# Performance work log

Measured on AMD Instinct MI355X. Metric: run time of the kernel, lower is better.

Reference implementation:

```python
import jax, jax.numpy as jnp
import numpy as np

HIDDEN = 2048
KEY_DIM = 2048
NUM_HEADS = 16
EPS = 1e-05


def rms_norm(x, w, eps=EPS):
    ms = jnp.mean(x * x, axis=-1, keepdims=True)
    return x * jax.lax.rsqrt(ms + eps) * w


def setup_inputs() -> dict:
    key = jax.random.key(0)
    ks = jax.random.split(key, 6)
    bound = 1.0 / np.sqrt(HIDDEN)  # kaiming-uniform-ish scale
    x = jax.random.normal(ks[0], (2, 2048, HIDDEN), dtype=jnp.float32)
    rms_w = jnp.ones((HIDDEN,), dtype=jnp.float32)
    Wq = jax.random.uniform(ks[1], (HIDDEN, KEY_DIM), jnp.float32, -bound, bound)
    Wk = jax.random.uniform(ks[2], (HIDDEN, KEY_DIM), jnp.float32, -bound, bound)
    Wv = jax.random.uniform(ks[3], (HIDDEN, KEY_DIM), jnp.float32, -bound, bound)
    Wo = jax.random.uniform(ks[4], (KEY_DIM, HIDDEN), jnp.float32, -bound, bound)
    return {"x": x, "rms_w": rms_w, "Wq": Wq, "Wk": Wk, "Wv": Wv, "Wo": Wo}


def reference(x, rms_w, Wq, Wk, Wv, Wo):
    B, S, _ = x.shape
    residual = x
    xn = rms_norm(x, rms_w)
    # project and split heads: [B,S,H,Dh]
    q = (xn @ Wq).reshape(B, S, NUM_HEADS, KEY_DIM // NUM_HEADS)
    k = (xn @ Wk).reshape(B, S, NUM_HEADS, KEY_DIM // NUM_HEADS)
    v = (xn @ Wv).reshape(B, S, NUM_HEADS, KEY_DIM // NUM_HEADS)
    # NOTE: original scales by 1/sqrt(key_dim), not head_dim — kept faithful
    scale = 1.0 / jnp.sqrt(jnp.float32(KEY_DIM))
    scores = jnp.einsum('bshd,bthd->bhst', q, k) * scale  # [B,H,S,S]
    causal = jnp.tril(jnp.ones((S, S), dtype=bool))
    scores = jnp.where(causal[None, None], scores, -jnp.inf)
    probs = jax.nn.softmax(scores, axis=-1)  # stable max-subtract internally
    out = jnp.einsum('bhst,bthd->bshd', probs, v).reshape(B, S, KEY_DIM)
    return out @ Wo + residual
```

## Files before the change

kernel.cpp:

```cpp
#include <hip/hip_runtime.h>
#include <math.h>

typedef __attribute__((ext_vector_type(8))) short bf16x8;
typedef __attribute__((ext_vector_type(4))) float f32x4;
typedef __attribute__((ext_vector_type(16))) float f32x16;

#define HID 2048
#define SEQ 2048
#define NH  16
#define DH  128
#define QS_LOG2E 0.0318793607f

__device__ __forceinline__ ushort f2bf(float f) {
  union { float f; unsigned u; } v; v.f = f;
  unsigned r = v.u + 0x7fffu + ((v.u >> 16) & 1u);
  return (ushort)(r >> 16);
}

__device__ __forceinline__ void gload16(const ushort* g, ushort* l) {
  __builtin_amdgcn_global_load_lds((const __attribute__((address_space(1))) void*)g,
                                   (__attribute__((address_space(3))) void*)l,
                                   16, 0, 0);
}

#define VMCNT(n) asm volatile("s_waitcnt vmcnt(" #n ")" ::: "memory")
#define ABAR()   asm volatile("s_barrier" ::: "memory")

__global__ __launch_bounds__(256) void k_prep(const float* __restrict__ W0,
                                              const float* __restrict__ W1,
                                              const float* __restrict__ W2,
                                              const float* __restrict__ W3,
                                              ushort* __restrict__ T0,
                                              ushort* __restrict__ T3,
                                              const float* __restrict__ x,
                                              const float* __restrict__ rw,
                                              ushort* __restrict__ xn) {
  const int z = blockIdx.z;
  if (z < 4) {
    __shared__ float t[32][33];
    const float* W = (z == 0) ? W0 : (z == 1) ? W1 : (z == 2) ? W2 : W3;
    ushort* Wt = (z == 3) ? T3 : (T0 + (size_t)z * 2048 * 2048);
    int n0 = blockIdx.x * 32, k0 = blockIdx.y * 32;
    int tx = threadIdx.x, ty = threadIdx.y;
    for (int i = ty; i < 32; i += 8)
      t[i][tx] = W[(size_t)(k0 + i) * HID + n0 + tx];
    __syncthreads();
    for (int i = ty; i < 32; i += 8)
      Wt[(size_t)(n0 + i) * HID + k0 + tx] = f2bf(t[tx][i]);
  } else {
    const int tid = threadIdx.y * 32 + threadIdx.x;
    const int row = blockIdx.y * 64 + blockIdx.x;
    const float* xr = x + (size_t)row * HID;
    int base = tid * 8;
    float4 a = *(const float4*)(xr + base);
    float4 c = *(const float4*)(xr + base + 4);
    float ss = a.x*a.x + a.y*a.y + a.z*a.z + a.w*a.w
             + c.x*c.x + c.y*c.y + c.z*c.z + c.w*c.w;
    #pragma unroll
    for (int off = 32; off > 0; off >>= 1) ss += __shfl_xor(ss, off);
    __shared__ float red[4];
    if ((tid & 63) == 0) red[tid >> 6] = ss;
    __syncthreads();
    float tot = red[0] + red[1] + red[2] + red[3];
    float sc = rsqrtf(tot * (1.0f / HID) + 1e-5f);
    float4 wa = *(const float4*)(rw + base);
    float4 wc = *(const float4*)(rw + base + 4);
    ushort h[8];
    h[0] = f2bf(a.x * sc * wa.x); h[1] = f2bf(a.y * sc * wa.y);
    h[2] = f2bf(a.z * sc * wa.z); h[3] = f2bf(a.w * sc * wa.w);
    h[4] = f2bf(c.x * sc * wc.x); h[5] = f2bf(c.y * sc * wc.y);
    h[6] = f2bf(c.z * sc * wc.z); h[7] = f2bf(c.w * sc * wc.w);
    int4 pk;
    pk.x = h[0] | ((int)h[1] << 16);
    pk.y = h[2] | ((int)h[3] << 16);
    pk.z = h[4] | ((int)h[5] << 16);
    pk.w = h[6] | ((int)h[7] << 16);
    *(int4*)&xn[(size_t)row * HID + base] = pk;
  }
}

__global__ __launch_bounds__(256, 2) void k_gemm12(const ushort* __restrict__ A,
                                                   const ushort* __restrict__ Bt,
                                                   ushort* __restrict__ obf,
                                                   ushort* __restrict__ vt) {
  constexpr int K = 2048, NR = 64;
  __shared__ ushort lds[4][8192];
  const int tid = threadIdx.x;
  const int lane = tid & 63, w = tid >> 6;
  const int wr = w >> 1, wc = w & 1;
  const int g = lane >> 4, l15 = lane & 15;
  const int bm = blockIdx.y, bn = blockIdx.x;

  f32x4 acc[4][4];
  #pragma unroll
  for (int i = 0; i < 4; ++i)
    #pragma unroll
    for (int j = 0; j < 4; ++j) acc[i][j] = f32x4{0.f, 0.f, 0.f, 0.f};

  const ushort* pA[2];
  const ushort* pB[2];
  #pragma unroll
  for (int L = 0; L < 2; ++L) {
    int row = L * 64 + (tid >> 2);
    int ck = (tid & 3) ^ ((row >> 1) & 3);
    pA[L] = &A[(size_t)(bm * 128 + row) * K + ck * 8];
    pB[L] = &Bt[(size_t)(bn * 128 + row) * K + ck * 8];
  }

  auto STAGE = [&](int slot) {
    ushort* base = lds[slot];
    #pragma unroll
    for (int L = 0; L < 2; ++L) {
      gload16(pA[L], base + L * 2048 + w * 512);
      pA[L] += 32;
    }
    #pragma unroll
    for (int L = 0; L < 2; ++L) {
      gload16(pB[L], base + 4096 + L * 2048 + w * 512);
      pB[L] += 32;
    }
  };

  auto COMP = [&](int slot) {
    const ushort* ra = lds[slot];
    const ushort* rb = ra + 4096;
    bf16x8 aF[4], bF[4];
    #pragma unroll
    for (int i = 0; i < 4; ++i) {
      int row = wr * 64 + i * 16 + l15;
      aF[i] = *(const bf16x8*)&ra[row * 32 + ((g ^ ((row >> 1) & 3)) * 8)];
    }
    #pragma unroll
    for (int j = 0; j < 4; ++j) {
      int row = wc * 64 + j * 16 + l15;
      bF[j] = *(const bf16x8*)&rb[row * 32 + ((g ^ ((row >> 1) & 3)) * 8)];
    }
    __builtin_amdgcn_s_setprio(1);
    #pragma unroll
    for (int i = 0; i < 4; ++i)
      #pragma unroll
      for (int j = 0; j < 4; ++j)
        acc[i][j] = __builtin_amdgcn_mfma_f32_16x16x32_bf16(aF[i], bF[j], acc[i][j], 0, 0, 0);
    __builtin_amdgcn_s_setprio(0);
  };

  STAGE(0); STAGE(1); STAGE(2);

  #pragma unroll 1
  for (int r = 0; r <= NR - 4; ++r) {
    VMCNT(8); ABAR();
    STAGE((r + 3) & 3);
    COMP(r & 3);
  }
  VMCNT(8); ABAR(); COMP((NR - 3) & 3);
  VMCNT(4); ABAR(); COMP((NR - 2) & 3);
  VMCNT(0); ABAR(); COMP((NR - 1) & 3);

  int rbase = bm * 128 + wr * 64 + g * 4;
  int cbase = bn * 128 + wc * 64 + l15;
  if (bn < 32) {
    const float sc = (bn < 16) ? QS_LOG2E : 1.0f;
    #pragma unroll
    for (int i = 0; i < 4; ++i) {
      #pragma unroll
      for (int j = 0; j < 4; ++j) {
        int col = cbase + j * 16;
        #pragma unroll
        for (int r = 0; r < 4; ++r) {
          int row = rbase + i * 16 + r;
          obf[(size_t)row * 4096 + col] = f2bf(acc[i][j][r] * sc);
        }
      }
    }
  } else {
    #pragma unroll
    for (int i = 0; i < 4; ++i) {
      int rowb = rbase + i * 16;
      int b = rowb >> 11, s = rowb & 2047;
      #pragma unroll
      for (int j = 0; j < 4; ++j) {
        int nv = cbase + j * 16 - 4096;
        int h = nv >> 7, d = nv & 127;
        uint lo = (uint)f2bf(acc[i][j][0]) | ((uint)f2bf(acc[i][j][1]) << 16);
        uint hi = (uint)f2bf(acc[i][j][2]) | ((uint)f2bf(acc[i][j][3]) << 16);
        uint2 pk = {lo, hi};
        *(uint2*)&vt[(size_t)((b * NH + h) * DH + d) * SEQ + s] = pk;
      }
    }
  }
}

__global__ __launch_bounds__(256) void k_gemm7o(const ushort* __restrict__ A,
                                                const ushort* __restrict__ Bt,
                                                float* __restrict__ ofl,
                                                const float* __restrict__ resid,
                                                int K) {
  __shared__ ushort sA[128 * 64];
  __shared__ ushort sB[128 * 64];
  const int tid = threadIdx.x;
  const int lane = tid & 63, w = tid >> 6;
  const int wr = w >> 1, wc = w & 1;
  const int bm = blockIdx.y, bn = blockIdx.x;
  const int g = lane >> 4, l15 = lane & 15;
  f32x4 acc[4][4];
  #pragma unroll
  for (int i = 0; i < 4; ++i)
    #pragma unroll
    for (int j = 0; j < 4; ++j) acc[i][j] = f32x4{0.f, 0.f, 0.f, 0.f};

  const ushort* ap[4];
  const ushort* bp[4];
  ushort* la[4];
  ushort* lb[4];
  #pragma unroll
  for (int c = 0; c < 4; ++c) {
    int id = (w * 4 + c) * 64 + lane;
    int r = id >> 3, ck = id & 7;
    int ke = (ck ^ (r & 7)) * 8;
    ap[c] = &A[(size_t)(bm * 128 + r) * K + ke];
    bp[c] = &Bt[(size_t)(bn * 128 + r) * K + ke];
    la[c] = ((ushort*)sA) + (w * 4 + c) * 512;
    lb[c] = ((ushort*)sB) + (w * 4 + c) * 512;
  }

  const int nt = K / 64;
  #pragma unroll 1
  for (int t = 0; t < nt; ++t) {
    #pragma unroll
    for (int c = 0; c < 4; ++c) {
      gload16(ap[c], la[c]);
      gload16(bp[c], lb[c]);
      ap[c] += 64;
      bp[c] += 64;
    }
    __syncthreads();
    #pragma unroll
    for (int kk = 0; kk < 2; ++kk) {
      bf16x8 aF[4], bF[4];
      #pragma unroll
      for (int i = 0; i < 4; ++i) {
        int row = wr * 64 + i * 16 + l15;
        int cp = (kk * 4 + g) ^ (lane & 7);
        aF[i] = *(const bf16x8*)&sA[row * 64 + cp * 8];
      }
      #pragma unroll
      for (int j = 0; j < 4; ++j) {
        int row = wc * 64 + j * 16 + l15;
        int cp = (kk * 4 + g) ^ (lane & 7);
        bF[j] = *(const bf16x8*)&sB[row * 64 + cp * 8];
      }
      #pragma unroll
      for (int i = 0; i < 4; ++i)
        #pragma unroll
        for (int j = 0; j < 4; ++j)
          acc[i][j] = __builtin_amdgcn_mfma_f32_16x16x32_bf16(aF[i], bF[j], acc[i][j], 0, 0, 0);
    }
    __syncthreads();
  }

  int rbase = bm * 128 + wr * 64 + g * 4;
  int cbase = bn * 128 + wc * 64 + l15;
  #pragma unroll
  for (int i = 0; i < 4; ++i) {
    #pragma unroll
    for (int j = 0; j < 4; ++j) {
      int col = cbase + j * 16;
      #pragma unroll
      for (int r = 0; r < 4; ++r) {
        int row = rbase + i * 16 + r;
        ofl[(size_t)row * HID + col] = acc[i][j][r] + resid[(size_t)row * HID + col];
      }
    }
  }
}

__global__ __launch_bounds__(256, 2) void k_attn6(const ushort* __restrict__ qk,
                                                  const ushort* __restrict__ vt,
                                                  ushort* __restrict__ aout) {
  __shared__ ushort sK[2][64 * 128];
  __shared__ ushort sV[2][128 * 64];
  const int tid = threadIdx.x;
  const int lane = tid & 63, w = tid >> 6;
  const int h2 = lane >> 5;
  const int l31 = lane & 31;
  const int bid = blockIdx.x;
  const int t = bid >> 3;
  const int u = t & 31, v = t >> 5;
  const int bh = (bid & 7) + 8 * (u & 3);
  const int qblk = v ? 15 - (u >> 2) : (u >> 2);
  const int b = bh >> 4, hh = bh & 15;
  const int q0w = qblk * 128 + w * 32;

  bf16x8 qf[8];
  {
    const ushort* qbase = qk + (size_t)(b * SEQ + q0w + l31) * 4096 + hh * DH;
    #pragma unroll
    for (int kk = 0; kk < 8; ++kk) qf[kk] = *(const bf16x8*)&qbase[kk * 16 + h2 * 8];
  }

  const ushort* kp[4];
  const ushort* vp[4];
  int lofs[4];
  #pragma unroll
  for (int c = 0; c < 4; ++c) {
    int id = (w * 4 + c) * 64 + lane;
    int kr = id >> 4, ck = id & 15;
    kp[c] = qk + (size_t)(b * SEQ + kr) * 4096 + 2048 + hh * DH + ((ck ^ (kr & 7)) * 8);
    int dr = id >> 3, cv = id & 7;
    vp[c] = vt + (size_t)(bh * DH + dr) * SEQ + ((cv ^ (dr & 7)) * 8);
    lofs[c] = (w * 4 + c) * 512;
  }

  auto STAGE = [&](int buf) {
    #pragma unroll
    for (int c = 0; c < 4; ++c) {
      gload16(kp[c], &sK[buf][0] + lofs[c]);
      gload16(vp[c], &sV[buf][0] + lofs[c]);
      kp[c] += 64 * 4096;
      vp[c] += 64;
    }
  };

  f32x16 accO[4];
  #pragma unroll
  for (int i = 0; i < 4; ++i)
    #pragma unroll
    for (int r = 0; r < 16; ++r) accO[i][r] = 0.f;
  float l_r = 0.f;

  auto COMPUTE = [&](int tt, int buf) {
    const int t0 = tt * 64;
    f32x16 accS[2];
    #pragma unroll
    for (int i = 0; i < 2; ++i)
      #pragma unroll
      for (int r = 0; r < 16; ++r) accS[i][r] = 0.f;
    #pragma unroll
    for (int kt = 0; kt < 2; ++kt) {
      const int row = kt * 32 + l31;
      #pragma unroll
      for (int kk = 0; kk < 8; ++kk) {
        const int cp = (kk * 2 + h2) ^ (lane & 7);
        bf16x8 kf = *(const bf16x8*)&sK[buf][row * 128 + cp * 8];
        accS[kt] = __builtin_amdgcn_mfma_f32_32x32x16_bf16(kf, qf[kk], accS[kt], 0, 0, 0);
      }
    }
    float rs = 0.f;
    if (t0 + 63 <= q0w) {
      #pragma unroll
      for (int kt = 0; kt < 2; ++kt)
        #pragma unroll
        for (int r = 0; r < 16; ++r) {
          float p = __builtin_amdgcn_exp2f(accS[kt][r]);
          rs += p;
          accS[kt][r] = p;
        }
    } else {
      const int qa = q0w + l31;
      #pragma unroll
      for (int kt = 0; kt < 2; ++kt)
        #pragma unroll
        for (int r = 0; r < 16; ++r) {
          int ka = t0 + kt * 32 + (r & 3) + 8 * (r >> 2) + 4 * h2;
          float p = (ka <= qa) ? __builtin_amdgcn_exp2f(accS[kt][r]) : 0.f;
          rs += p;
          accS[kt][r] = p;
        }
    }
    rs += __shfl_xor(rs, 32);
    l_r += rs;

    uint W[2][4][2];
    #pragma unroll
    for (int kt = 0; kt < 2; ++kt)
      #pragma unroll
      for (int bq = 0; bq < 4; ++bq)
        #pragma unroll
        for (int w2 = 0; w2 < 2; ++w2) {
          uint u0 = __float_as_uint(accS[kt][bq * 4 + w2 * 2]);
          uint u1 = __float_as_uint(accS[kt][bq * 4 + w2 * 2 + 1]);
          W[kt][bq][w2] = (u0 >> 16) | (u1 & 0xffff0000u);
        }
    #pragma unroll
    for (int kc = 0; kc < 4; ++kc) {
      const int kt = kc >> 1, pq = kc & 1;
      uint X0 = W[kt][2 * pq][0],     X1 = W[kt][2 * pq][1];
      uint Y0 = W[kt][2 * pq + 1][0], Y1 = W[kt][2 * pq + 1][1];
      uint sx0 = (uint)__shfl_xor((int)X0, 32);
      uint sx1 = (uint)__shfl_xor((int)X1, 32);
      uint sy0 = (uint)__shfl_xor((int)Y0, 32);
      uint sy1 = (uint)__shfl_xor((int)Y1, 32);
      union { uint u[4]; bf16x8 v; } pu;
      pu.u[0] = h2 ? sy0 : X0;
      pu.u[1] = h2 ? sy1 : X1;
      pu.u[2] = h2 ? Y0 : sx0;
      pu.u[3] = h2 ? Y1 : sx1;
      #pragma unroll
      for (int ds = 0; ds < 4; ++ds) {
        const int dr = ds * 32 + l31;
        const int cp = (kc * 2 + h2) ^ (lane & 7);
        bf16x8 vf = *(const bf16x8*)&sV[buf][dr * 64 + cp * 8];
        accO[ds] = __builtin_amdgcn_mfma_f32_32x32x16_bf16(pu.v, vf, accO[ds], 0, 0, 0);
      }
    }
  };

  const int ntile = 2 * qblk + 2;
  STAGE(0);
  #pragma unroll 1
  for (int tt = 0; tt < ntile - 1; ++tt) {
    STAGE((tt + 1) & 1);
    VMCNT(8);
    ABAR();
    if (tt * 64 <= q0w + 31) COMPUTE(tt, tt & 1);
    ABAR();
  }
  VMCNT(0);
  ABAR();
  if ((ntile - 1) * 64 <= q0w + 31) COMPUTE(ntile - 1, (ntile - 1) & 1);

  float linv = 1.f / l_r;
  #pragma unroll
  for (int r = 0; r < 16; ++r) {
    int qrel = (r & 3) + 8 * (r >> 2) + 4 * h2;
    float li = __shfl(linv, qrel);
    #pragma unroll
    for (int ds = 0; ds < 4; ++ds) {
      aout[(size_t)(b * SEQ + q0w + qrel) * HID + hh * DH + ds * 32 + l31] =
          f2bf(accO[ds][r] * li);
    }
  }
}

extern "C" void kernel_launch(void* const* d_in, const int* in_sizes, int n_in,
                              void* d_out, int out_size, void* d_ws, size_t ws_size,
                              hipStream_t stream) {
  const float* x     = (const float*)d_in[0];
  const float* rms_w = (const float*)d_in[1];
  const float* Wq    = (const float*)d_in[2];
  const float* Wk    = (const float*)d_in[3];
  const float* Wv    = (const float*)d_in[4];
  const float* Wo    = (const float*)d_in[5];
  float* out = (float*)d_out;

  char* ws = (char*)d_ws;
  ushort* WqkvT = (ushort*)ws; ws += (size_t)6144 * 2048 * 2;
  ushort* WoT   = (ushort*)ws; ws += (size_t)2048 * 2048 * 2;
  ushort* xn    = (ushort*)ws; ws += (size_t)4096 * 2048 * 2;
  ushort* qkbuf = (ushort*)ws; ws += (size_t)4096 * 4096 * 2;
  ushort* vt    = (ushort*)ws; ws += (size_t)4096 * 2048 * 2;
  ushort* aout  = (ushort*)ws; ws += (size_t)4096 * 2048 * 2;

  k_prep<<<dim3(64, 64, 5), dim3(32, 8), 0, stream>>>(Wq, Wk, Wv, Wo, WqkvT, WoT,
                                                      x, rms_w, xn);

  k_gemm12<<<dim3(48, 32), 256, 0, stream>>>(xn, WqkvT, qkbuf, vt);

  k_attn6<<<512, 256, 0, stream>>>(qkbuf, vt, aout);

  k_gemm7o<<<dim3(16, 32), 256, 0, stream>>>(aout, WoT, out, x, 2048);
}
```

Baseline: 254.8 us.

## Use 3-stage pipelined GEMM with 3 blocks/CU for both QKV and output projections

The QKV GEMM pipeline drops from four LDS stages to three, and its launch bound rises to three blocks per CU for more occupancy. The output projection GEMM, which was a simple single-buffered kernel, now reuses the same templated pipelined kernel, with a MODE switch for the fp32 residual epilogue. This aims to hide memory latency better in both GEMMs. The trade-off is a shallower prefetch depth and more register pressure from the 3-block bound.

New measurement: 254.9 us. No clear change (+0.0%).

```diff
diff --git a/kernel.cpp b/kernel.cpp
--- a/kernel.cpp
+++ b/kernel.cpp
@@ -79,12 +79,15 @@
   }
 }
 
-__global__ __launch_bounds__(256, 2) void k_gemm12(const ushort* __restrict__ A,
+template <int MODE>
+__global__ __launch_bounds__(256, 3) void k_gemm13(const ushort* __restrict__ A,
                                                    const ushort* __restrict__ Bt,
                                                    ushort* __restrict__ obf,
-                                                   ushort* __restrict__ vt) {
+                                                   ushort* __restrict__ vt,
+                                                   float* __restrict__ ofl,
+                                                   const float* __restrict__ resid) {
   constexpr int K = 2048, NR = 64;
-  __shared__ ushort lds[4][8192];
+  __shared__ ushort lds[3][8192];
   const int tid = threadIdx.x;
   const int lane = tid & 63, w = tid >> 6;
   const int wr = w >> 1, wc = w & 1;
@@ -144,21 +147,33 @@
     __builtin_amdgcn_s_setprio(0);
   };
 
-  STAGE(0); STAGE(1); STAGE(2);
+  STAGE(0); STAGE(1);
 
   #pragma unroll 1
-  for (int r = 0; r <= NR - 4; ++r) {
-    VMCNT(8); ABAR();
-    STAGE((r + 3) & 3);
-    COMP(r & 3);
-  }
-  VMCNT(8); ABAR(); COMP((NR - 3) & 3);
-  VMCNT(4); ABAR(); COMP((NR - 2) & 3);
-  VMCNT(0); ABAR(); COMP((NR - 1) & 3);
+  for (int r = 0; r <= NR - 3; ++r) {
+    VMCNT(4); ABAR();
+    STAGE((r + 2) % 3);
+    COMP(r % 3);
+  }
+  VMCNT(4); ABAR(); COMP((NR - 2) % 3);
+  VMCNT(0); ABAR(); COMP((NR - 1) % 3);
 
   int rbase = bm * 128 + wr * 64 + g * 4;
   int cbase = bn * 128 + wc * 64 + l15;
-  if (bn < 32) {
+  if (MODE == 1) {
+    #pragma unroll
+    for (int i = 0; i < 4; ++i) {
+      #pragma unroll
+      for (int j = 0; j < 4; ++j) {
+        int col = cbase + j * 16;
+        #pragma unroll
+        for (int r = 0; r < 4; ++r) {
+          int row = rbase + i * 16 + r;
+          ofl[(size_t)row * HID + col] = acc[i][j][r] + resid[(size_t)row * HID + col];
+        }
+      }
+    }
+  } else if (bn < 32) {
     const float sc = (bn < 16) ? QS_LOG2E : 1.0f;
     #pragma unroll
     for (int i = 0; i < 4; ++i) {
@@ -185,90 +200,6 @@
         uint hi = (uint)f2bf(acc[i][j][2]) | ((uint)f2bf(acc[i][j][3]) << 16);
         uint2 pk = {lo, hi};
         *(uint2*)&vt[(size_t)((b * NH + h) * DH + d) * SEQ + s] = pk;
-      }
-    }
-  }
-}
-
-__global__ __launch_bounds__(256) void k_gemm7o(const ushort* __restrict__ A,
-                                                const ushort* __restrict__ Bt,
-                                                float* __restrict__ ofl,
-                                                const float* __restrict__ resid,
-                                                int K) {
-  __shared__ ushort sA[128 * 64];
-  __shared__ ushort sB[128 * 64];
-  const int tid = threadIdx.x;
-  const int lane = tid & 63, w = tid >> 6;
-  const int wr = w >> 1, wc = w & 1;
-  const int bm = blockIdx.y, bn = blockIdx.x;
-  const int g = lane >> 4, l15 = lane & 15;
-  f32x4 acc[4][4];
-  #pragma unroll
-  for (int i = 0; i < 4; ++i)
-    #pragma unroll
-    for (int j = 0; j < 4; ++j) acc[i][j] = f32x4{0.f, 0.f, 0.f, 0.f};
-
-  const ushort* ap[4];
-  const ushort* bp[4];
-  ushort* la[4];
-  ushort* lb[4];
-  #pragma unroll
-  for (int c = 0; c < 4; ++c) {
-    int id = (w * 4 + c) * 64 + lane;
-    int r = id >> 3, ck = id & 7;
-    int ke = (ck ^ (r & 7)) * 8;
-    ap[c] = &A[(size_t)(bm * 128 + r) * K + ke];
-    bp[c] = &Bt[(size_t)(bn * 128 + r) * K + ke];
-    la[c] = ((ushort*)sA) + (w * 4 + c) * 512;
-    lb[c] = ((ushort*)sB) + (w * 4 + c) * 512;
-  }
-
-  const int nt = K / 64;
-  #pragma unroll 1
-  for (int t = 0; t < nt; ++t) {
-    #pragma unroll
-    for (int c = 0; c < 4; ++c) {
-      gload16(ap[c], la[c]);
-      gload16(bp[c], lb[c]);
-      ap[c] += 64;
-      bp[c] += 64;
-    }
-    __syncthreads();
-    #pragma unroll
-    for (int kk = 0; kk < 2; ++kk) {
-      bf16x8 aF[4], bF[4];
-      #pragma unroll
-      for (int i = 0; i < 4; ++i) {
-        int row = wr * 64 + i * 16 + l15;
-        int cp = (kk * 4 + g) ^ (lane & 7);
-        aF[i] = *(const bf16x8*)&sA[row * 64 + cp * 8];
-      }
-      #pragma unroll
-      for (int j = 0; j < 4; ++j) {
-        int row = wc * 64 + j * 16 + l15;
-        int cp = (kk * 4 + g) ^ (lane & 7);
-        bF[j] = *(const bf16x8*)&sB[row * 64 + cp * 8];
-      }
-      #pragma unroll
-      for (int i = 0; i < 4; ++i)
-        #pragma unroll
-        for (int j = 0; j < 4; ++j)
-          acc[i][j] = __builtin_amdgcn_mfma_f32_16x16x32_bf16(aF[i], bF[j], acc[i][j], 0, 0, 0);
-    }
-    __syncthreads();
-  }
-
-  int rbase = bm * 128 + wr * 64 + g * 4;
-  int cbase = bn * 128 + wc * 64 + l15;
-  #pragma unroll
-  for (int i = 0; i < 4; ++i) {
-    #pragma unroll
-    for (int j = 0; j < 4; ++j) {
-      int col = cbase + j * 16;
-      #pragma unroll
-      for (int r = 0; r < 4; ++r) {
-        int row = rbase + i * 16 + r;
-        ofl[(size_t)row * HID + col] = acc[i][j][r] + resid[(size_t)row * HID + col];
       }
     }
   }
@@ -454,9 +385,9 @@
   k_prep<<<dim3(64, 64, 5), dim3(32, 8), 0, stream>>>(Wq, Wk, Wv, Wo, WqkvT, WoT,
                                                       x, rms_w, xn);
 
-  k_gemm12<<<dim3(48, 32), 256, 0, stream>>>(xn, WqkvT, qkbuf, vt);
+  k_gemm13<0><<<dim3(48, 32), 256, 0, stream>>>(xn, WqkvT, qkbuf, vt, nullptr, nullptr);
 
   k_attn6<<<512, 256, 0, stream>>>(qkbuf, vt, aout);
 
-  k_gemm7o<<<dim3(16, 32), 256, 0, stream>>>(aout, WoT, out, x, 2048);
-}
+  k_gemm13<1><<<dim3(16, 32), 256, 0, stream>>>(aout, WoT, nullptr, nullptr, out, x);
+}
```
